# Optimization experiments

Hardware: AMD Instinct MI355X
Metric: run time of the kernel (lower is better)

Reference implementation:

```python
import jax, jax.numpy as jnp
import numpy as np

MUL = 128      # multiplicity of 0e and 1o irreps
K = 4          # number of node-attr scalar channels (elements)
DIM = MUL + MUL * 3  # 512 flattened irrep dim


def setup_inputs() -> dict:
    key = jax.random.key(0)
    k1, k2, k3, k4, k5, k6, k7 = jax.random.split(key, 7)
    N = 100000
    m_i = jax.random.normal(k1, (N, DIM), dtype=jnp.float32)
    node_feats = jax.random.normal(k2, (N, DIM), dtype=jnp.float32)
    node_attrs = jax.random.uniform(k3, (N, K), dtype=jnp.float32)
    # o3.Linear internal weights: one [mul_in, mul_out] block per irrep (0e, 1o)
    W_lin0 = jax.random.normal(k4, (MUL, MUL), dtype=jnp.float32)
    W_lin1 = jax.random.normal(k5, (MUL, MUL), dtype=jnp.float32)
    # FullyConnectedTensorProduct weights: one [u, v, w] tensor per path
    # paths: (0e x 0e -> 0e) and (1o x 0e -> 1o); CG for l x 0 -> l is identity
    W_tp0 = jax.random.normal(k6, (MUL, K, MUL), dtype=jnp.float32)
    W_tp1 = jax.random.normal(k7, (MUL, K, MUL), dtype=jnp.float32)
    return {"m_i": m_i, "node_feats": node_feats, "node_attrs": node_attrs,
            "W_lin0": W_lin0, "W_lin1": W_lin1, "W_tp0": W_tp0, "W_tp1": W_tp1}


def _split(x):
    # [N, 512] -> ([N, 128] scalars, [N, 128, 3] vectors)
    s = x[:, :MUL]
    v = x[:, MUL:].reshape(x.shape[0], MUL, 3)
    return s, v


def reference(m_i, node_feats, node_attrs, W_lin0, W_lin1, W_tp0, W_tp1):
    N = m_i.shape[0]
    inv_lin = 1.0 / np.sqrt(MUL)          # e3nn Linear path normalization (fan_in = mul_in)
    inv_tp = 1.0 / np.sqrt(MUL * K)       # FCTP path normalization (fan_in = mul1*mul2)

    m0, m1 = _split(m_i)
    f0, f1 = _split(node_feats)

    # o3.Linear on hidden irreps: block-diagonal per-irrep matmul over multiplicity
    lin0 = (m0 @ W_lin0) * inv_lin                               # [N, 128]
    lin1 = jnp.einsum('num,uw->nwm', m1, W_lin1) * inv_lin       # [N, 128, 3]

    # FullyConnectedTensorProduct(feats, attrs): attrs are 0e scalars so CG is trivial
    tp0 = jnp.einsum('nu,nv,uvw->nw', f0, node_attrs, W_tp0) * inv_tp        # [N, 128]
    tp1 = jnp.einsum('num,nv,uvw->nwm', f1, node_attrs, W_tp1) * inv_tp      # [N, 128, 3]

    out0 = lin0 + tp0
    out1 = (lin1 + tp1).reshape(N, MUL * 3)
    return jnp.concatenate([out0, out1], axis=1)  # [N, 512]
```

## Files before the change

kernel.cpp:

```cpp
#include <hip/hip_runtime.h>


#define MUL 128
#define DIM 512
#define KTOT 640
#define NSTEPS 20
#define NODES 16
#define INV_LIN 0.08838834764831845f
#define INV_TP  0.04419417382415922f

typedef float f32x4 __attribute__((ext_vector_type(4)));
typedef __bf16 bf16x8 __attribute__((ext_vector_type(8)));

__device__ inline unsigned short f2bf(float x) {
    unsigned u = __float_as_uint(x);
    u += 0x7fffu + ((u >> 16) & 1u);
    return (unsigned short)(u >> 16);
}

__global__ __launch_bounds__(256) void prep_weights(
        const float* __restrict__ Wl0, const float* __restrict__ Wl1,
        const float* __restrict__ Wt0, const float* __restrict__ Wt1,
        unsigned short* __restrict__ P0, unsigned short* __restrict__ P1) {
    int idx = blockIdx.x * 256 + threadIdx.x;
    if (idx >= 2 * MUL * KTOT) return;
    int mat = idx / (MUL * KTOT);
    int r   = idx % (MUL * KTOT);
    int w = r / KTOT, k = r % KTOT;
    const float* Wl = mat ? Wl1 : Wl0;
    const float* Wt = mat ? Wt1 : Wt0;
    float val;
    if (k < MUL) {
        val = Wl[k * MUL + w] * INV_LIN;
    } else {
        int kk = k - MUL;
        val = Wt[(kk >> 2) * 512 + (kk & 3) * 128 + w] * INV_TP;
    }
    int ct = w >> 5, ct2 = (w >> 4) & 1, lr = w & 15;
    int ks = k >> 5, g = (k >> 3) & 3, i = k & 7;
    (mat ? P1 : P0)[((((ct * NSTEPS + ks) * 2 + ct2) * 64 + g * 16 + lr) << 3) + i] = f2bf(val);
}

#define POOL_BYTES 34816
__global__ __launch_bounds__(256, 4) void k_fused(
        const float* __restrict__ m_i, const float* __restrict__ nf,
        const float* __restrict__ attrs,
        const bf16x8* __restrict__ P0, const bf16x8* __restrict__ P1,
        float* __restrict__ out, int N) {
    __shared__ __align__(16) char pool[POOL_BYTES];
    __bf16 (*Mde)[NODES][136] = (__bf16(*)[NODES][136])(pool);
    __bf16 (*Fde)[NODES][136] = (__bf16(*)[NODES][136])(pool + 17408);

    int tid = threadIdx.x;
    int ct = tid >> 6, l = tid & 63;
    int lr = l & 15, g = l >> 4;

    long nodeBase = (long)blockIdx.x * NODES;

    for (int c = tid; c < NODES * 128; c += 256) {
        int nl = c >> 7, q = c & 127;
        long node = nodeBase + nl; if (node >= N) node = N - 1;
        f32x4 x = *(const f32x4*)&m_i[node * DIM + q * 4];
        f32x4 y = *(const f32x4*)&nf [node * DIM + q * 4];
        #pragma unroll
        for (int j = 0; j < 4; ++j) {
            int col = q * 4 + j;
            int cls, u;
            if (col < 128) { cls = 0; u = col; }
            else { int cc = col - 128; cls = 1 + cc % 3; u = cc / 3; }
            Mde[cls][nl][u] = (__bf16)x[j];
            Fde[cls][nl][u] = (__bf16)y[j];
        }
    }

    long nA = nodeBase + lr; if (nA >= N) nA = N - 1;
    f32x4 at = *(const f32x4*)&attrs[nA * 4];

    f32x4 acc[4][2] = {};
    __syncthreads();

    #pragma unroll
    for (int ks = 0; ks < 4; ++ks) {
        bf16x8 b0[2], b1[2];
        #pragma unroll
        for (int c2 = 0; c2 < 2; ++c2) {
            b0[c2] = P0[((ct * NSTEPS + ks) * 2 + c2) * 64 + l];
            b1[c2] = P1[((ct * NSTEPS + ks) * 2 + c2) * 64 + l];
        }
        #pragma unroll
        for (int cls = 0; cls < 4; ++cls) {
            bf16x8 af = *(const bf16x8*)&Mde[cls][lr][ks * 32 + g * 8];
            #pragma unroll
            for (int c2 = 0; c2 < 2; ++c2)
                acc[cls][c2] = __builtin_amdgcn_mfma_f32_16x16x32_bf16(
                    af, cls ? b1[c2] : b0[c2], acc[cls][c2], 0, 0, 0);
        }
    }
    #pragma unroll 2
    for (int ks = 4; ks < NSTEPS; ++ks) {
        bf16x8 b0[2], b1[2];
        #pragma unroll
        for (int c2 = 0; c2 < 2; ++c2) {
            b0[c2] = P0[((ct * NSTEPS + ks) * 2 + c2) * 64 + l];
            b1[c2] = P1[((ct * NSTEPS + ks) * 2 + c2) * 64 + l];
        }
        int u0 = (ks - 4) * 8 + g * 2;
        #pragma unroll
        for (int cls = 0; cls < 4; ++cls) {
            float fx = (float)Fde[cls][lr][u0];
            float fy = (float)Fde[cls][lr][u0 + 1];
            bf16x8 a;
            a[0]=(__bf16)(fx*at[0]); a[1]=(__bf16)(fx*at[1]);
            a[2]=(__bf16)(fx*at[2]); a[3]=(__bf16)(fx*at[3]);
            a[4]=(__bf16)(fy*at[0]); a[5]=(__bf16)(fy*at[1]);
            a[6]=(__bf16)(fy*at[2]); a[7]=(__bf16)(fy*at[3]);
            #pragma unroll
            for (int c2 = 0; c2 < 2; ++c2)
                acc[cls][c2] = __builtin_amdgcn_mfma_f32_16x16x32_bf16(
                    a, cls ? b1[c2] : b0[c2], acc[cls][c2], 0, 0, 0);
        }
    }

    __syncthreads();
    float (*Ost)[DIM] = (float(*)[DIM])pool;
    #pragma unroll
    for (int c2 = 0; c2 < 2; ++c2) {
        int wv_ = ct * 32 + c2 * 16 + lr;
        #pragma unroll
        for (int r = 0; r < 4; ++r) {
            int nl = g * 4 + r;
            Ost[nl][wv_]               = acc[0][c2][r];
            Ost[nl][128 + wv_ * 3 + 0] = acc[1][c2][r];
            Ost[nl][128 + wv_ * 3 + 1] = acc[2][c2][r];
            Ost[nl][128 + wv_ * 3 + 2] = acc[3][c2][r];
        }
    }
    __syncthreads();
    for (int c = tid; c < NODES * 128; c += 256) {
        int nl = c >> 7, q = c & 127;
        long node = nodeBase + nl;
        if (node < N)
            *(f32x4*)&out[node * DIM + q * 4] = *(const f32x4*)&Ost[nl][q * 4];
    }
}

extern "C" void kernel_launch(void* const* d_in, const int* in_sizes, int n_in,
                              void* d_out, int out_size, void* d_ws, size_t ws_size,
                              hipStream_t stream) {
    const float* m_i  = (const float*)d_in[0];
    const float* nf   = (const float*)d_in[1];
    const float* attr = (const float*)d_in[2];
    const float* Wl0  = (const float*)d_in[3];
    const float* Wl1  = (const float*)d_in[4];
    const float* Wt0  = (const float*)d_in[5];
    const float* Wt1  = (const float*)d_in[6];
    float* out = (float*)d_out;
    int N = in_sizes[0] / DIM;

    unsigned short* P0 = (unsigned short*)d_ws;
    unsigned short* P1 = P0 + MUL * KTOT;

    int prep_total = 2 * MUL * KTOT;
    hipLaunchKernelGGL(prep_weights, dim3((prep_total + 255) / 256), dim3(256), 0, stream,
                       Wl0, Wl1, Wt0, Wt1, P0, P1);
    hipLaunchKernelGGL(k_fused, dim3((N + NODES - 1) / NODES), dim3(256), 0, stream,
                       m_i, nf, attr, (const bf16x8*)P0, (const bf16x8*)P1, out, N);
}
```

Baseline: 198.7 us.

## Factor node attrs out of TP GEMM, apply per-attr scaling in epilogue

Restructures the tensor-product part: instead of building the A operand by multiplying each feature by every attribute inside the inner loop, it runs four plain GEMMs (one per attribute channel) on the unmodified bf16 features. Each result is then scaled by that node's attribute in fp32 and added to the accumulator. The weight packing is reordered so the K dimension is grouped by attribute channel. This removes the per-step scalar LDS loads, multiplies and bf16 conversions, and lets the feature operand use vector LDS reads. In exchange it adds temporary accumulators (register pressure) and extra FMA epilogue work.

```diff
diff --git a/kernel.cpp b/kernel.cpp
--- a/kernel.cpp
+++ b/kernel.cpp
@@ -29,12 +29,12 @@
     int w = r / KTOT, k = r % KTOT;
     const float* Wl = mat ? Wl1 : Wl0;
     const float* Wt = mat ? Wt1 : Wt0;
+    int sec = k >> 7, u = k & 127;
     float val;
-    if (k < MUL) {
-        val = Wl[k * MUL + w] * INV_LIN;
+    if (sec == 0) {
+        val = Wl[u * MUL + w] * INV_LIN;
     } else {
-        int kk = k - MUL;
-        val = Wt[(kk >> 2) * 512 + (kk & 3) * 128 + w] * INV_TP;
+        val = Wt[u * 512 + (sec - 1) * 128 + w] * INV_TP;
     }
     int ct = w >> 5, ct2 = (w >> 4) & 1, lr = w & 15;
     int ks = k >> 5, g = (k >> 3) & 3, i = k & 7;
@@ -73,8 +73,12 @@
         }
     }
 
-    long nA = nodeBase + lr; if (nA >= N) nA = N - 1;
-    f32x4 at = *(const f32x4*)&attrs[nA * 4];
+    f32x4 at_row[4];
+    #pragma unroll
+    for (int r = 0; r < 4; ++r) {
+        long nd = nodeBase + g * 4 + r; if (nd >= N) nd = N - 1;
+        at_row[r] = *(const f32x4*)&attrs[nd * 4];
+    }
 
     f32x4 acc[4][2] = {};
     __syncthreads();
@@ -96,29 +100,35 @@
                     af, cls ? b1[c2] : b0[c2], acc[cls][c2], 0, 0, 0);
         }
     }
-    #pragma unroll 2
-    for (int ks = 4; ks < NSTEPS; ++ks) {
-        bf16x8 b0[2], b1[2];
+
+    #pragma unroll
+    for (int v = 0; v < 4; ++v) {
+        f32x4 tmp[4][2] = {};
         #pragma unroll
-        for (int c2 = 0; c2 < 2; ++c2) {
-            b0[c2] = P0[((ct * NSTEPS + ks) * 2 + c2) * 64 + l];
-            b1[c2] = P1[((ct * NSTEPS + ks) * 2 + c2) * 64 + l];
+        for (int ks = 0; ks < 4; ++ks) {
+            int kst = (1 + v) * 4 + ks;
+            bf16x8 b0[2], b1[2];
+            #pragma unroll
+            for (int c2 = 0; c2 < 2; ++c2) {
+                b0[c2] = P0[((ct * NSTEPS + kst) * 2 + c2) * 64 + l];
+                b1[c2] = P1[((ct * NSTEPS + kst) * 2 + c2) * 64 + l];
+            }
+            #pragma unroll
+            for (int cls = 0; cls < 4; ++cls) {
+                bf16x8 af = *(const bf16x8*)&Fde[cls][lr][ks * 32 + g * 8];
+                #pragma unroll
+                for (int c2 = 0; c2 < 2; ++c2)
+                    tmp[cls][c2] = __builtin_amdgcn_mfma_f32_16x16x32_bf16(
+                        af, cls ? b1[c2] : b0[c2], tmp[cls][c2], 0, 0, 0);
+            }
         }
-        int u0 = (ks - 4) * 8 + g * 2;
         #pragma unroll
-        for (int cls = 0; cls < 4; ++cls) {
-            float fx = (float)Fde[cls][lr][u0];
-            float fy = (float)Fde[cls][lr][u0 + 1];
-            bf16x8 a;
-            a[0]=(__bf16)(fx*at[0]); a[1]=(__bf16)(fx*at[1]);
-            a[2]=(__bf16)(fx*at[2]); a[3]=(__bf16)(fx*at[3]);
-            a[4]=(__bf16)(fy*at[0]); a[5]=(__bf16)(fy*at[1]);
-            a[6]=(__bf16)(fy*at[2]); a[7]=(__bf16)(fy*at[3]);
+        for (int cls = 0; cls < 4; ++cls)
             #pragma unroll
             for (int c2 = 0; c2 < 2; ++c2)
-                acc[cls][c2] = __builtin_amdgcn_mfma_f32_16x16x32_bf16(
-                    a, cls ? b1[c2] : b0[c2], acc[cls][c2], 0, 0, 0);
-        }
+                #pragma unroll
+                for (int r = 0; r < 4; ++r)
+                    acc[cls][c2][r] += at_row[r][v] * tmp[cls][c2][r];
     }
 
     __syncthreads();
```

Result: slower. 493.3 us (+148.3%).
